# Optimization experiments

Measured on AMD Instinct MI355X. Metric: run time of the kernel, lower is better.

## Reference

```python
import jax, jax.numpy as jnp
import numpy as np

B, T = 128, 512
V, E, H, A, L = 50000, 256, 512, 64, 2


def setup_inputs() -> dict:
    key = jax.random.key(0)
    ks = jax.random.split(key, 16)
    token_ids = jax.random.randint(ks[0], (B, T), 0, V, dtype=jnp.int32)
    # lengths must be >= 2 so that the source's (len-1)-1 index is valid
    lengths = jnp.clip(jax.random.randint(ks[1], (B,), 0, T, dtype=jnp.int32), 4, T)
    s = 0.05
    inp = {
        "token_ids": token_ids,
        "lengths": lengths,
        "embedding": jax.random.normal(ks[2], (V, E), jnp.float32) * s,
        "Wt": jax.random.normal(ks[3], (A, E), jnp.float32) * s,   # tokens_linear
        "bt": jax.random.normal(ks[4], (A,), jnp.float32) * s,
        "Wq": jax.random.normal(ks[5], (A, H), jnp.float32) * s,   # query_linear
        "bq": jax.random.normal(ks[6], (A,), jnp.float32) * s,
        "v": jax.random.normal(ks[7], (A,), jnp.float32) * s,      # attention_linear weight
        "bv": jax.random.normal(ks[8], (), jnp.float32) * s,       # attention_linear bias
        "gru_Wih0": jax.random.normal(ks[9], (3 * H, A), jnp.float32) * s,
        "gru_Whh0": jax.random.normal(ks[10], (3 * H, H), jnp.float32) * s,
        "gru_bih0": jax.random.normal(ks[11], (3 * H,), jnp.float32) * s,
        "gru_bhh0": jax.random.normal(ks[12], (3 * H,), jnp.float32) * s,
        "gru_Wih1": jax.random.normal(ks[13], (3 * H, H), jnp.float32) * s,
        "gru_Whh1": jax.random.normal(ks[14], (3 * H, H), jnp.float32) * s,
        "gru_bih1": jax.random.normal(ks[15], (3 * H,), jnp.float32) * s,
        "gru_bhh1": jax.random.normal(jax.random.fold_in(key, 99), (3 * H,), jnp.float32) * s,
    }
    return inp


def _gru_cell(x, h, Wih, Whh, bih, bhh):
    gi = x @ Wih.T + bih      # [B, 3H]
    gh = h @ Whh.T + bhh      # [B, 3H]
    i_r, i_z, i_n = jnp.split(gi, 3, axis=-1)
    h_r, h_z, h_n = jnp.split(gh, 3, axis=-1)
    r = jax.nn.sigmoid(i_r + h_r)
    z = jax.nn.sigmoid(i_z + h_z)
    n = jnp.tanh(i_n + r * h_n)
    return (1.0 - z) * n + z * h


def reference(token_ids, lengths, embedding, Wt, bt, Wq, bq, v, bv,
              gru_Wih0, gru_Whh0, gru_bih0, gru_bhh0,
              gru_Wih1, gru_Whh1, gru_bih1, gru_bhh1):
    x = embedding[token_ids]                 # [B, T, E]
    tp = jnp.einsum('bte,ae->bta', x, Wt) + bt   # tokens_linear, [B, T, A]
    pos = jnp.arange(T)

    def step(h, i):
        # query = hidden_state[-1] (zeros at step 0, matching hidden_state=None)
        q = h[-1] @ Wq.T + bq                # [B, A]
        s = jnp.tanh(tp + q[:, None, :]) @ v + bv   # [B, T]
        s = jnp.where(pos[None, :] <= i, s, -jnp.inf)  # growing prefix
        attn = jax.nn.softmax(s, axis=1)
        ctx = jnp.einsum('bt,bta->ba', attn, tp)     # [B, A]
        h0 = _gru_cell(ctx, h[0], gru_Wih0, gru_Whh0, gru_bih0, gru_bhh0)
        h1 = _gru_cell(h0, h[1], gru_Wih1, gru_Whh1, gru_bih1, gru_bhh1)
        return jnp.stack([h0, h1]), h1

    h_init = jnp.zeros((L, B, H), tp.dtype)
    _, outs = jax.lax.scan(step, h_init, jnp.arange(T))   # outs: [T, B, H]
    # source: sequence_lengths = len-1, then index sequence_lengths-1 = len-2
    idx = jnp.clip(lengths - 2, 0, T - 1)
    result = outs[idx, jnp.arange(B)]                     # [B, H]
    return result
```

## Files before the change

### kernel.cpp

```cpp
#include <hip/hip_runtime.h>

#define NB 128
#define NT 512
#define NE 256
#define NH 512
#define NA 64
#define NG 8
#define GB 16

typedef short bf16x8 __attribute__((ext_vector_type(8)));
typedef float f32x4 __attribute__((ext_vector_type(4)));
typedef unsigned short u16x8 __attribute__((ext_vector_type(8)));
typedef unsigned long long u64;

__device__ __forceinline__ unsigned short f2bf(float f){
  unsigned u = __builtin_bit_cast(unsigned, f);
  u = u + 0x7fffu + ((u >> 16) & 1u);
  return (unsigned short)(u >> 16);
}
__device__ __forceinline__ float bf2f(unsigned short h){
  unsigned u = ((unsigned)h) << 16;
  return __builtin_bit_cast(float, u);
}
__device__ __forceinline__ bf16x8 packbf2(f32x4 a, f32x4 b){
  bf16x8 r;
  r[0]=(short)f2bf(a[0]); r[1]=(short)f2bf(a[1]); r[2]=(short)f2bf(a[2]); r[3]=(short)f2bf(a[3]);
  r[4]=(short)f2bf(b[0]); r[5]=(short)f2bf(b[1]); r[6]=(short)f2bf(b[2]); r[7]=(short)f2bf(b[3]);
  return r;
}
__device__ __forceinline__ bf16x8 loadB_f32(const float* p){
  f32x4 a = *(const f32x4*)p;
  f32x4 b = *(const f32x4*)(p + 4);
  return packbf2(a, b);
}
#define MFMA(a,b,c) __builtin_amdgcn_mfma_f32_16x16x32_bf16(a,b,c,0,0,0)

__device__ __forceinline__ float fsig(float x){
  return __builtin_amdgcn_rcpf(1.f + __expf(-x));
}
__device__ __forceinline__ float ftanh(float x){
  float e2 = __expf(2.f * x);
  return 1.f - 2.f * __builtin_amdgcn_rcpf(e2 + 1.f);
}

__device__ __forceinline__ void sleep_bk(int bk){
  if (bk <= 0)      __builtin_amdgcn_s_sleep(1);
  else if (bk == 1) __builtin_amdgcn_s_sleep(2);
  else if (bk == 2) __builtin_amdgcn_s_sleep(4);
  else              __builtin_amdgcn_s_sleep(8);
}

__device__ __forceinline__ u64 aload(const u64* p){
  return __hip_atomic_load(p, __ATOMIC_RELAXED, __HIP_MEMORY_SCOPE_AGENT);
}
__device__ __forceinline__ void fire(u64* p, u64 v){
  (void)__hip_atomic_exchange(p, v, __ATOMIC_RELAXED, __HIP_MEMORY_SCOPE_AGENT);
}
__device__ __forceinline__ u64 packh(unsigned sq, float a, float b){
  return ((u64)sq << 32) | ((u64)f2bf(b) << 16) | (u64)f2bf(a);
}
__device__ __forceinline__ u64 packf(unsigned sq, float a){
  return ((u64)sq << 32) | (u64)__builtin_bit_cast(unsigned, a);
}

__global__ __launch_bounds__(256) void k_tp(
    const int* __restrict__ tok, const float* __restrict__ emb,
    const float* __restrict__ Wt, const float* __restrict__ bt,
    unsigned short* __restrict__ tp)
{
  const int lane = threadIdx.x & 63;
  const int w = threadIdx.x >> 6;
  const int m16 = lane & 15, quad = lane >> 4;

  bf16x8 wfq[8][4];
#pragma unroll
  for (int kc = 0; kc < 8; kc++)
#pragma unroll
    for (int nt = 0; nt < 4; nt++)
      wfq[kc][nt] = loadB_f32(Wt + (nt*16 + m16)*NE + kc*32 + quad*8);

  float btv[4];
#pragma unroll
  for (int nt = 0; nt < 4; nt++) btv[nt] = bt[nt*16 + m16];

  const int gw = blockIdx.x * 4 + w;
#pragma unroll 1
  for (int it = 0; it < 4; it++){
    const int pt = gw * 4 + it;
    const int pos = pt*16 + m16;
    const long row = (long)tok[pos];
    const float* xrow = emb + row * NE;
    f32x4 acc[4] = {{0,0,0,0},{0,0,0,0},{0,0,0,0},{0,0,0,0}};
#pragma unroll
    for (int kc = 0; kc < 8; kc++){
      bf16x8 af = loadB_f32(xrow + kc*32 + quad*8);
#pragma unroll
      for (int nt = 0; nt < 4; nt++)
        acc[nt] = MFMA(af, wfq[kc][nt], acc[nt]);
    }
#pragma unroll
    for (int nt = 0; nt < 4; nt++)
#pragma unroll
      for (int r = 0; r < 4; r++){
        int posr = pt*16 + quad*4 + r;
        tp[(long)posr * NA + nt*16 + m16] = f2bf(acc[nt][r] + btv[nt]);
      }
  }
}

__global__ __launch_bounds__(256) void k_pack(
    const float* __restrict__ Wq, unsigned short* __restrict__ blob)
{
  const int lane = threadIdx.x & 63, wv = threadIdx.x >> 6;
  const int m16 = lane & 15, quad = lane >> 4;
#pragma unroll
  for (int kc = 0; kc < 16; kc++){
    bf16x8 t = loadB_f32(Wq + (long)(wv*16 + m16)*NH + kc*32 + quad*8);
    *(bf16x8*)&blob[((wv*16 + kc)*64 + lane)*8] = t;
  }
}

struct KArgs {
  const int* len;
  const float* bq; const float* v; const float* bv;
  const float* Wih0; const float* Whh0; const float* bih0; const float* bhh0;
  const float* Wih1; const float* Whh1; const float* bih1; const float* bhh1;
  const unsigned short* tp;
  const unsigned short* wqblob;
  u64* hbuf;
  u64* cbuf;
  float* out;
};

__device__ __forceinline__ void stage_load(const u64* __restrict__ buf, unsigned sq,
                                           unsigned short (*hs)[64][8], int tid){
  const int lane = tid & 63, wv = tid >> 6;
  const int b = lane & 15, q8 = lane >> 4;
  u64 x[16];
  int bk = 0;
  for (;;){
    bool ok = true;
#pragma unroll
    for (int c = 0; c < 4; c++){
      const u64* u0 = buf + ((wv*4 + c)*4 + q8)*64 + b*4;
#pragma unroll
      for (int j = 0; j < 4; j++) x[c*4 + j] = aload(u0 + j);
    }
#pragma unroll
    for (int t = 0; t < 16; t++) ok &= ((unsigned)(x[t] >> 32) == sq);
    if (ok) break;
    sleep_bk(bk);
    if (bk < 3) bk++;
  }
#pragma unroll
  for (int c = 0; c < 4; c++){
    u16x8 d;
#pragma unroll
    for (int j = 0; j < 4; j++){
      d[2*j]   = (unsigned short)x[c*4 + j];
      d[2*j+1] = (unsigned short)(x[c*4 + j] >> 16);
    }
    *(u16x8*)&hs[wv*4 + c][lane][0] = d;
  }
}

__global__ __launch_bounds__(256, 1) void k_main(KArgs A_)
{
  const int tid = threadIdx.x, lane = tid & 63, w = tid >> 6;
  const int g = blockIdx.x & 7, m = blockIdx.x >> 3;
  const int m16 = lane & 15, quad = lane >> 4;

  __shared__ __attribute__((aligned(16))) unsigned short h0s[16][64][8];
  __shared__ __attribute__((aligned(16))) unsigned short h1s[16][64][8];
  __shared__ __attribute__((aligned(16))) float dslab[6][256];
  __shared__ __attribute__((aligned(16))) float qs[16][68];
  __shared__ __attribute__((aligned(16))) float cslab[4][64];
  __shared__ float cden[4];
  __shared__ __attribute__((aligned(16))) unsigned short ctxf[64][16];

  u64* hb = A_.hbuf + (long)g * (4*4096);
  u64* cb = A_.cbuf + (long)g * (2*2*16*72);
  const int b0 = g * GB;

  bf16x8 wf[48], wih0f[2];
  float bhh0v[4], bih0v[4], bhh1v[4], bih1v[4];
  if (w < 3){
    const int r0 = w * NH + m * 16;
#pragma unroll
    for (int kc = 0; kc < 16; kc++){
      wf[kc]    = loadB_f32(A_.Whh0 + (long)(r0 + m16)*NH + kc*32 + quad*8);
      wf[16+kc] = loadB_f32(A_.Whh1 + (long)(r0 + m16)*NH + kc*32 + quad*8);
      wf[32+kc] = loadB_f32(A_.Wih1 + (long)(r0 + m16)*NH + kc*32 + quad*8);
    }
#pragma unroll
    for (int kc = 0; kc < 2; kc++)
      wih0f[kc] = loadB_f32(A_.Wih0 + (r0 + m16)*NA + kc*32 + quad*8);
#pragma unroll
    for (int r = 0; r < 4; r++){
      int d = r0 + quad*4 + r;
      bhh0v[r] = A_.bhh0[d]; bih0v[r] = A_.bih0[d];
      bhh1v[r] = A_.bhh1[d]; bih1v[r] = A_.bih1[d];
    }
  }
  float bqw[4];
#pragma unroll
  for (int r = 0; r < 4; r++) bqw[r] = A_.bq[w*16 + quad*4 + r];

  float vv[16];
#pragma unroll
  for (int jj = 0; jj < 16; jj++) vv[jj] = A_.v[quad*16 + jj];
  const float bvv = A_.bv[0];
  const int ab = m >> 1;
  const int wr = (m & 1)*4 + w;

  int myidx = 0, imax = 0;
#pragma unroll 1
  for (int b = 0; b < GB; b++){
    int L = A_.len[b0 + b];
    int ix = L - 2; ix = ix < 0 ? 0 : (ix > NT-1 ? NT-1 : ix);
    if (b == m16) myidx = ix;
    imax = imax > ix ? imax : ix;
  }

  f32x4 h0p = {0,0,0,0}, h1p = {0,0,0,0};

  {
    u16x8 z = {0,0,0,0,0,0,0,0};
#pragma unroll
    for (int c = 0; c < 4; c++){
      int kc = (tid>>6)*4 + c;
      *(u16x8*)&h0s[kc][lane][0] = z;
      *(u16x8*)&h1s[kc][lane][0] = z;
    }
  }
  __syncthreads();

#pragma unroll 1
  for (int i = 0; i <= imax; i++){
    const int par = i & 1;
    const unsigned sq = (unsigned)(i + 1);

    f32x4 g0 = {0,0,0,0};
    if (w < 3){
#pragma unroll
      for (int kc = 0; kc < 16; kc++){
        bf16x8 h0f = *(const bf16x8*)&h0s[kc][lane][0];
        g0 = MFMA(wf[kc], h0f, g0);
      }
#pragma unroll
      for (int r = 0; r < 4; r++) g0[r] += bhh0v[r];
    }
    if (i > 0){
      stage_load(hb + (long)(2 + ((i-1)&1))*4096, (unsigned)i, h1s, tid);
      __syncthreads();
    }
    {
      f32x4 qa = {0,0,0,0};
#pragma unroll
      for (int kc = 0; kc < 16; kc++){
        bf16x8 b1f = *(const bf16x8*)&h1s[kc][lane][0];
        bf16x8 af = *(const bf16x8*)&A_.wqblob[((w*16 + kc)*64 + lane)*8];
        qa = MFMA(af, b1f, qa);
      }
#pragma unroll
      for (int r = 0; r < 4; r++)
        qs[m16][w*16 + quad*4 + r] = qa[r] + bqw[r];
    }
    __syncthreads();

    {
      float qv[16];
#pragma unroll
      for (int jq = 0; jq < 4; jq++){
        f32x4 t = *(const f32x4*)&qs[ab][quad*16 + jq*4];
        qv[jq*4+0]=t[0]; qv[jq*4+1]=t[1]; qv[jq*4+2]=t[2]; qv[jq*4+3]=t[3];
      }
      float ctxp[16];
#pragma unroll
      for (int jj = 0; jj < 16; jj++) ctxp[jj] = 0.f;
      float denp = 0.f;
      const unsigned short* tpb = A_.tp + (long)(b0 + ab) * NT * NA;
#pragma unroll 1
      for (int c = wr; c*16 <= i; c += 8){
        const int t = c*16 + m16;
        const unsigned short* tpp = tpb + (long)t*NA + quad*16;
        u16x8 ta = *(const u16x8*)tpp;
        u16x8 tb = *(const u16x8*)(tpp + 8);
        float tpf[16];
#pragma unroll
        for (int jj = 0; jj < 8; jj++){ tpf[jj] = bf2f(ta[jj]); tpf[8+jj] = bf2f(tb[jj]); }
        float sp = 0.f;
#pragma unroll
        for (int jj = 0; jj < 16; jj++){
          float x = tpf[jj] + qv[jj];
          sp = fmaf(ftanh(x), vv[jj], sp);
        }
        sp += __shfl_xor(sp, 16);
        sp += __shfl_xor(sp, 32);
        float e = __expf(sp + bvv);
        e = (t <= i) ? e : 0.f;
        denp += e;
#pragma unroll
        for (int jj = 0; jj < 16; jj++) ctxp[jj] = fmaf(e, tpf[jj], ctxp[jj]);
      }
#pragma unroll
      for (int off = 1; off < 64; off <<= 1) denp += __shfl_xor(denp, off);
      denp *= 0.25f;
#pragma unroll
      for (int st = 0; st < 4; st++){
        const int bit = 1 << st;
        const bool up = (lane >> st) & 1;
        const int n2 = (16 >> st) >> 1;
#pragma unroll
        for (int j2 = 0; j2 < 8; j2++){
          if (j2 < n2){
            float keep = up ? ctxp[2*j2+1] : ctxp[2*j2];
            float send = up ? ctxp[2*j2]   : ctxp[2*j2+1];
            float got = __shfl_xor(send, bit);
            ctxp[j2] = keep + got;
          }
        }
      }
      cslab[w][lane] = ctxp[0];
      if (lane == 0) cden[w] = denp;
    }
    __syncthreads();
    if (w == 0){
      float s = cslab[0][lane] + cslab[1][lane] + cslab[2][lane] + cslab[3][lane];
      u64* slot = cb + ((long)(par*2 + (m & 1))*16 + ab)*72;
      fire(slot + lane, packf(sq, s));
      if (lane == 0)
        fire(slot + 64, packf(sq, cden[0]+cden[1]+cden[2]+cden[3]));
    }

    if (w == 3){
      const u64* c0 = cb + ((long)(par*2 + 0)*16 + m16)*72;
      const u64* c1 = cb + ((long)(par*2 + 1)*16 + m16)*72;
      u64 d0, d1, t0[16], t1[16];
      int bk = 0;
      for (;;){
        bool ok = true;
        d0 = aload(c0 + 64); d1 = aload(c1 + 64);
#pragma unroll
        for (int kc = 0; kc < 2; kc++){
          const int a0 = kc*32 + quad*8;
#pragma unroll
          for (int j = 0; j < 8; j++){
            t0[kc*8 + j] = aload(c0 + a0 + j);
            t1[kc*8 + j] = aload(c1 + a0 + j);
          }
        }
        ok = ((unsigned)(d0>>32) == sq) & ((unsigned)(d1>>32) == sq);
#pragma unroll
        for (int t = 0; t < 16; t++)
          ok &= ((unsigned)(t0[t]>>32) == sq) & ((unsigned)(t1[t]>>32) == sq);
        if (ok) break;
        sleep_bk(bk);
        if (bk < 3) bk++;
      }
      const float rdn = __builtin_amdgcn_rcpf(
          __builtin_bit_cast(float,(unsigned)d0) + __builtin_bit_cast(float,(unsigned)d1));
#pragma unroll
      for (int kc = 0; kc < 2; kc++){
        u16x8 f;
#pragma unroll
        for (int j = 0; j < 8; j++){
          float s = (__builtin_bit_cast(float,(unsigned)t0[kc*8+j]) +
                     __builtin_bit_cast(float,(unsigned)t1[kc*8+j])) * rdn;
          f[j] = f2bf(s);
        }
        *(u16x8*)&ctxf[lane][kc*8] = f;
      }
    }
    __syncthreads();
    if (w < 3){
      f32x4 gi0 = {0,0,0,0};
      bf16x8 cf0 = *(const bf16x8*)&ctxf[lane][0];
      bf16x8 cf1 = *(const bf16x8*)&ctxf[lane][8];
      gi0 = MFMA(wih0f[0], cf0, gi0);
      gi0 = MFMA(wih0f[1], cf1, gi0);
#pragma unroll
      for (int r = 0; r < 4; r++) gi0[r] += bih0v[r];
      *(f32x4*)&dslab[w][lane*4] = g0;
      *(f32x4*)&dslab[3+w][lane*4] = gi0;
    }
    __syncthreads();
    if (w == 3){
      f32x4 ghr = *(f32x4*)&dslab[0][lane*4];
      f32x4 ghz = *(f32x4*)&dslab[1][lane*4];
      f32x4 ghn = *(f32x4*)&dslab[2][lane*4];
      f32x4 gir = *(f32x4*)&dslab[3][lane*4];
      f32x4 giz = *(f32x4*)&dslab[4][lane*4];
      f32x4 gin = *(f32x4*)&dslab[5][lane*4];
      f32x4 hn;
#pragma unroll
      for (int r = 0; r < 4; r++){
        float rr = fsig(gir[r] + ghr[r]);
        float zz = fsig(giz[r] + ghz[r]);
        float nn = ftanh(gin[r] + rr*ghn[r]);
        hn[r] = (1.f - zz)*nn + zz*h0p[r];
      }
      h0p = hn;
      const int dp0 = m*8 + quad*2;
      u64* p0 = hb + (long)par*4096 + (dp0>>2)*64 + m16*4 + (dp0&3);
      fire(p0,     packh(sq, hn[0], hn[1]));
      fire(p0 + 1, packh(sq, hn[2], hn[3]));
    }

    f32x4 gh1 = {0,0,0,0};
    if (w < 3){
#pragma unroll
      for (int kc = 0; kc < 16; kc++){
        bf16x8 b1f = *(const bf16x8*)&h1s[kc][lane][0];
        gh1 = MFMA(wf[16+kc], b1f, gh1);
      }
#pragma unroll
      for (int r = 0; r < 4; r++) gh1[r] += bhh1v[r];
    }
    stage_load(hb + (long)par*4096, sq, h0s, tid);
    __syncthreads();
    if (w < 3){
      f32x4 gi1 = {0,0,0,0};
#pragma unroll
      for (int kc = 0; kc < 16; kc++){
        bf16x8 hf = *(const bf16x8*)&h0s[kc][lane][0];
        gi1 = MFMA(wf[32+kc], hf, gi1);
      }
#pragma unroll
      for (int r = 0; r < 4; r++) gi1[r] += bih1v[r];
      *(f32x4*)&dslab[w][lane*4] = gh1;
      *(f32x4*)&dslab[3+w][lane*4] = gi1;
    }
    __syncthreads();
    if (w == 3){
      f32x4 ghr = *(f32x4*)&dslab[0][lane*4];
      f32x4 ghz = *(f32x4*)&dslab[1][lane*4];
      f32x4 ghn = *(f32x4*)&dslab[2][lane*4];
      f32x4 gir = *(f32x4*)&dslab[3][lane*4];
      f32x4 giz = *(f32x4*)&dslab[4][lane*4];
      f32x4 gin = *(f32x4*)&dslab[5][lane*4];
      f32x4 hn;
#pragma unroll
      for (int r = 0; r < 4; r++){
        float rr = fsig(gir[r] + ghr[r]);
        float zz = fsig(giz[r] + ghz[r]);
        float nn = ftanh(gin[r] + rr*ghn[r]);
        hn[r] = (1.f - zz)*nn + zz*h1p[r];
      }
      h1p = hn;
      const int dp0 = m*8 + quad*2;
      u64* p1 = hb + (long)(2 + par)*4096 + (dp0>>2)*64 + m16*4 + (dp0&3);
      fire(p1,     packh(sq, hn[0], hn[1]));
      fire(p1 + 1, packh(sq, hn[2], hn[3]));
      if (i == myidx)
        *(f32x4*)&A_.out[(long)(b0 + m16)*NH + m*16 + quad*4] = hn;
    }
  }
}

extern "C" void kernel_launch(void* const* d_in, const int* in_sizes, int n_in,
                              void* d_out, int out_size, void* d_ws, size_t ws_size,
                              hipStream_t stream)
{
  (void)in_sizes; (void)n_in; (void)out_size; (void)ws_size;
  char* ws = (char*)d_ws;
  unsigned short* tp     = (unsigned short*)ws;
  unsigned short* wqblob = (unsigned short*)(ws + 8388608);
  u64* hbuf = (u64*)(ws + 8388608 + 65536);
  u64* cbuf = hbuf + 8 * (4*4096);

  (void)hipMemsetAsync(hbuf, 0xFF, (size_t)(8*4*4096 + 8*2*2*16*72) * sizeof(u64), stream);

  k_tp<<<dim3(256), dim3(256), 0, stream>>>(
      (const int*)d_in[0], (const float*)d_in[2], (const float*)d_in[3],
      (const float*)d_in[4], tp);
  k_pack<<<dim3(1), dim3(256), 0, stream>>>((const float*)d_in[5], wqblob);

  KArgs ka;
  ka.len  = (const int*)d_in[1];
  ka.bq   = (const float*)d_in[6];
  ka.v    = (const float*)d_in[7];  ka.bv   = (const float*)d_in[8];
  ka.Wih0 = (const float*)d_in[9];  ka.Whh0 = (const float*)d_in[10];
  ka.bih0 = (const float*)d_in[11]; ka.bhh0 = (const float*)d_in[12];
  ka.Wih1 = (const float*)d_in[13]; ka.Whh1 = (const float*)d_in[14];
  ka.bih1 = (const float*)d_in[15]; ka.bhh1 = (const float*)d_in[16];
  ka.tp = tp; ka.wqblob = wqblob;
  ka.hbuf = hbuf; ka.cbuf = cbuf;
  ka.out = (float*)d_out;

  k_main<<<dim3(256), dim3(256), 0, stream>>>(ka);
}
```

Measured before the change: 7.737 ms.

## Split each batch group into two interleaved half-batches to overlap recurrence stages

Each block now processes two half-batch sub-groups (A and B, 8 sequences each) in an interleaved software pipeline, so one sub-group's attention and cross-block exchange can overlap the other's GRU work. The layer-0 hidden matmul is moved to after the h0 exchange and computed alongside the layer-1 input matmul. Exchange buffers are resized and a simpler per-thread 8-word staging load is used. This adds more barriers per step, duplicated code and extra register pressure, and uses only half the lanes in some phases.

```diff
diff --git a/kernel.cpp b/kernel.cpp
--- a/kernel.cpp
+++ b/kernel.cpp
@@ -132,36 +132,25 @@
   float* out;
 };
 
-__device__ __forceinline__ void stage_load(const u64* __restrict__ buf, unsigned sq,
-                                           unsigned short (*hs)[64][8], int tid){
-  const int lane = tid & 63, wv = tid >> 6;
-  const int b = lane & 15, q8 = lane >> 4;
-  u64 x[16];
+__device__ __forceinline__ void stage8(const u64* __restrict__ buf, unsigned sq,
+                                       unsigned short (*hs)[64][8], int tid){
+  const u64* u0 = buf + (long)tid * 8;
+  u64 x[8];
   int bk = 0;
   for (;;){
     bool ok = true;
 #pragma unroll
-    for (int c = 0; c < 4; c++){
-      const u64* u0 = buf + ((wv*4 + c)*4 + q8)*64 + b*4;
-#pragma unroll
-      for (int j = 0; j < 4; j++) x[c*4 + j] = aload(u0 + j);
-    }
-#pragma unroll
-    for (int t = 0; t < 16; t++) ok &= ((unsigned)(x[t] >> 32) == sq);
+    for (int j = 0; j < 8; j++) x[j] = aload(u0 + j);
+#pragma unroll
+    for (int j = 0; j < 8; j++) ok &= ((unsigned)(x[j] >> 32) == sq);
     if (ok) break;
     sleep_bk(bk);
     if (bk < 3) bk++;
   }
-#pragma unroll
-  for (int c = 0; c < 4; c++){
-    u16x8 d;
-#pragma unroll
-    for (int j = 0; j < 4; j++){
-      d[2*j]   = (unsigned short)x[c*4 + j];
-      d[2*j+1] = (unsigned short)(x[c*4 + j] >> 16);
-    }
-    *(u16x8*)&hs[wv*4 + c][lane][0] = d;
-  }
+  const int kc = tid >> 4, q8 = (tid >> 2) & 3, e0 = (tid & 3) * 2;
+#pragma unroll
+  for (int b = 0; b < 8; b++)
+    *(unsigned*)&hs[kc][q8*16 + b][e0] = (unsigned)x[b];
 }
 
 __global__ __launch_bounds__(256, 1) void k_main(KArgs A_)
@@ -170,16 +159,20 @@
   const int g = blockIdx.x & 7, m = blockIdx.x >> 3;
   const int m16 = lane & 15, quad = lane >> 4;
 
-  __shared__ __attribute__((aligned(16))) unsigned short h0s[16][64][8];
-  __shared__ __attribute__((aligned(16))) unsigned short h1s[16][64][8];
+  __shared__ __attribute__((aligned(16))) unsigned short h0sA[16][64][8];
+  __shared__ __attribute__((aligned(16))) unsigned short h1sA[16][64][8];
+  __shared__ __attribute__((aligned(16))) unsigned short h0sB[16][64][8];
+  __shared__ __attribute__((aligned(16))) unsigned short h1sB[16][64][8];
   __shared__ __attribute__((aligned(16))) float dslab[6][256];
   __shared__ __attribute__((aligned(16))) float qs[16][68];
   __shared__ __attribute__((aligned(16))) float cslab[4][64];
   __shared__ float cden[4];
   __shared__ __attribute__((aligned(16))) unsigned short ctxf[64][16];
 
-  u64* hb = A_.hbuf + (long)g * (4*4096);
-  u64* cb = A_.cbuf + (long)g * (2*2*16*72);
+  u64* hbA = A_.hbuf + ((long)g*2 + 0) * (4*2048);
+  u64* hbB = A_.hbuf + ((long)g*2 + 1) * (4*2048);
+  u64* cbA = A_.cbuf + ((long)g*2 + 0) * (2*2*16*72);
+  u64* cbB = A_.cbuf + ((long)g*2 + 1) * (2*2*16*72);
   const int b0 = g * GB;
 
   bf16x8 wf[48], wih0f[2];
@@ -210,27 +203,35 @@
 #pragma unroll
   for (int jj = 0; jj < 16; jj++) vv[jj] = A_.v[quad*16 + jj];
   const float bvv = A_.bv[0];
-  const int ab = m >> 1;
+  const int abl = (m >> 1) & 7;
   const int wr = (m & 1)*4 + w;
-
-  int myidx = 0, imax = 0;
+  const bool ownA = (m < 16), ownB = (m >= 16);
+
+  int myidxA = 0, myidxB = 0, imax = 0;
 #pragma unroll 1
   for (int b = 0; b < GB; b++){
     int L = A_.len[b0 + b];
     int ix = L - 2; ix = ix < 0 ? 0 : (ix > NT-1 ? NT-1 : ix);
-    if (b == m16) myidx = ix;
+    if (b == m16)     myidxA = ix;
+    if (b == m16 + 8) myidxB = ix;
     imax = imax > ix ? imax : ix;
   }
 
-  f32x4 h0p = {0,0,0,0}, h1p = {0,0,0,0};
+  f32x4 h0pA = {0,0,0,0}, h1pA = {0,0,0,0};
+  f32x4 h0pB = {0,0,0,0}, h1pB = {0,0,0,0};
+  f32x4 gh0cA = {0,0,0,0}, gh0cB = {0,0,0,0};
+  if (w < 3){
+#pragma unroll
+    for (int r = 0; r < 4; r++){ gh0cA[r] = bhh0v[r]; gh0cB[r] = bhh0v[r]; }
+  }
 
   {
     u16x8 z = {0,0,0,0,0,0,0,0};
 #pragma unroll
     for (int c = 0; c < 4; c++){
-      int kc = (tid>>6)*4 + c;
-      *(u16x8*)&h0s[kc][lane][0] = z;
-      *(u16x8*)&h1s[kc][lane][0] = z;
+      int kc = w*4 + c;
+      *(u16x8*)&h0sA[kc][lane][0] = z; *(u16x8*)&h1sA[kc][lane][0] = z;
+      *(u16x8*)&h0sB[kc][lane][0] = z; *(u16x8*)&h1sB[kc][lane][0] = z;
     }
   }
   __syncthreads();
@@ -239,26 +240,15 @@
   for (int i = 0; i <= imax; i++){
     const int par = i & 1;
     const unsigned sq = (unsigned)(i + 1);
-
-    f32x4 g0 = {0,0,0,0};
-    if (w < 3){
+    f32x4 gh1A = {0,0,0,0}, gh1B = {0,0,0,0};
+
+    if (i > 0) stage8(hbA + (long)(2 + ((i-1)&1))*2048, (unsigned)i, h1sA, tid);
+    __syncthreads();
+    if (ownA){
+      f32x4 qa = {0,0,0,0};
 #pragma unroll
       for (int kc = 0; kc < 16; kc++){
-        bf16x8 h0f = *(const bf16x8*)&h0s[kc][lane][0];
-        g0 = MFMA(wf[kc], h0f, g0);
-      }
-#pragma unroll
-      for (int r = 0; r < 4; r++) g0[r] += bhh0v[r];
-    }
-    if (i > 0){
-      stage_load(hb + (long)(2 + ((i-1)&1))*4096, (unsigned)i, h1s, tid);
-      __syncthreads();
-    }
-    {
-      f32x4 qa = {0,0,0,0};
-#pragma unroll
-      for (int kc = 0; kc < 16; kc++){
-        bf16x8 b1f = *(const bf16x8*)&h1s[kc][lane][0];
+        bf16x8 b1f = *(const bf16x8*)&h1sA[kc][lane][0];
         bf16x8 af = *(const bf16x8*)&A_.wqblob[((w*16 + kc)*64 + lane)*8];
         qa = MFMA(af, b1f, qa);
       }
@@ -267,19 +257,18 @@
         qs[m16][w*16 + quad*4 + r] = qa[r] + bqw[r];
     }
     __syncthreads();
-
-    {
+    if (ownA){
       float qv[16];
 #pragma unroll
       for (int jq = 0; jq < 4; jq++){
-        f32x4 t = *(const f32x4*)&qs[ab][quad*16 + jq*4];
+        f32x4 t = *(const f32x4*)&qs[abl][quad*16 + jq*4];
         qv[jq*4+0]=t[0]; qv[jq*4+1]=t[1]; qv[jq*4+2]=t[2]; qv[jq*4+3]=t[3];
       }
       float ctxp[16];
 #pragma unroll
       for (int jj = 0; jj < 16; jj++) ctxp[jj] = 0.f;
       float denp = 0.f;
-      const unsigned short* tpb = A_.tp + (long)(b0 + ab) * NT * NA;
+      const unsigned short* tpb = A_.tp + (long)(b0 + abl) * NT * NA;
 #pragma unroll 1
       for (int c = wr; c*16 <= i; c += 8){
         const int t = c*16 + m16;
@@ -325,17 +314,115 @@
       if (lane == 0) cden[w] = denp;
     }
     __syncthreads();
-    if (w == 0){
+    if (ownA && w == 0){
       float s = cslab[0][lane] + cslab[1][lane] + cslab[2][lane] + cslab[3][lane];
-      u64* slot = cb + ((long)(par*2 + (m & 1))*16 + ab)*72;
+      u64* slot = cbA + ((long)(par*2 + (m & 1))*16 + abl)*72;
       fire(slot + lane, packf(sq, s));
       if (lane == 0)
         fire(slot + 64, packf(sq, cden[0]+cden[1]+cden[2]+cden[3]));
     }
-
-    if (w == 3){
-      const u64* c0 = cb + ((long)(par*2 + 0)*16 + m16)*72;
-      const u64* c1 = cb + ((long)(par*2 + 1)*16 + m16)*72;
+    if (w < 3){
+#pragma unroll
+      for (int kc = 0; kc < 16; kc++){
+        bf16x8 b1f = *(const bf16x8*)&h1sA[kc][lane][0];
+        gh1A = MFMA(wf[16+kc], b1f, gh1A);
+      }
+#pragma unroll
+      for (int r = 0; r < 4; r++) gh1A[r] += bhh1v[r];
+    }
+
+    if (i > 0) stage8(hbB + (long)(2 + ((i-1)&1))*2048, (unsigned)i, h1sB, tid);
+    __syncthreads();
+    if (ownB){
+      f32x4 qa = {0,0,0,0};
+#pragma unroll
+      for (int kc = 0; kc < 16; kc++){
+        bf16x8 b1f = *(const bf16x8*)&h1sB[kc][lane][0];
+        bf16x8 af = *(const bf16x8*)&A_.wqblob[((w*16 + kc)*64 + lane)*8];
+        qa = MFMA(af, b1f, qa);
+      }
+#pragma unroll
+      for (int r = 0; r < 4; r++)
+        qs[m16][w*16 + quad*4 + r] = qa[r] + bqw[r];
+    }
+    __syncthreads();
+    if (ownB){
+      float qv[16];
+#pragma unroll
+      for (int jq = 0; jq < 4; jq++){
+        f32x4 t = *(const f32x4*)&qs[abl][quad*16 + jq*4];
+        qv[jq*4+0]=t[0]; qv[jq*4+1]=t[1]; qv[jq*4+2]=t[2]; qv[jq*4+3]=t[3];
+      }
+      float ctxp[16];
+#pragma unroll
+      for (int jj = 0; jj < 16; jj++) ctxp[jj] = 0.f;
+      float denp = 0.f;
+      const unsigned short* tpb = A_.tp + (long)(b0 + 8 + abl) * NT * NA;
+#pragma unroll 1
+      for (int c = wr; c*16 <= i; c += 8){
+        const int t = c*16 + m16;
+        const unsigned short* tpp = tpb + (long)t*NA + quad*16;
+        u16x8 ta = *(const u16x8*)tpp;
+        u16x8 tb = *(const u16x8*)(tpp + 8);
+        float tpf[16];
+#pragma unroll
+        for (int jj = 0; jj < 8; jj++){ tpf[jj] = bf2f(ta[jj]); tpf[8+jj] = bf2f(tb[jj]); }
+        float sp = 0.f;
+#pragma unroll
+        for (int jj = 0; jj < 16; jj++){
+          float x = tpf[jj] + qv[jj];
+          sp = fmaf(ftanh(x), vv[jj], sp);
+        }
+        sp += __shfl_xor(sp, 16);
+        sp += __shfl_xor(sp, 32);
+        float e = __expf(sp + bvv);
+        e = (t <= i) ? e : 0.f;
+        denp += e;
+#pragma unroll
+        for (int jj = 0; jj < 16; jj++) ctxp[jj] = fmaf(e, tpf[jj], ctxp[jj]);
+      }
+#pragma unroll
+      for (int off = 1; off < 64; off <<= 1) denp += __shfl_xor(denp, off);
+      denp *= 0.25f;
+#pragma unroll
+      for (int st = 0; st < 4; st++){
+        const int bit = 1 << st;
+        const bool up = (lane >> st) & 1;
+        const int n2 = (16 >> st) >> 1;
+#pragma unroll
+        for (int j2 = 0; j2 < 8; j2++){
+          if (j2 < n2){
+            float keep = up ? ctxp[2*j2+1] : ctxp[2*j2];
+            float send = up ? ctxp[2*j2]   : ctxp[2*j2+1];
+            float got = __shfl_xor(send, bit);
+            ctxp[j2] = keep + got;
+          }
+        }
+      }
+      cslab[w][lane] = ctxp[0];
+      if (lane == 0) cden[w] = denp;
+    }
+    __syncthreads();
+    if (ownB && w == 0){
+      float s = cslab[0][lane] + cslab[1][lane] + cslab[2][lane] + cslab[3][lane];
+      u64* slot = cbB + ((long)(par*2 + (m & 1))*16 + abl)*72;
+      fire(slot + lane, packf(sq, s));
+      if (lane == 0)
+        fire(slot + 64, packf(sq, cden[0]+cden[1]+cden[2]+cden[3]));
+    }
+    if (w < 3){
+#pragma unroll
+      for (int kc = 0; kc < 16; kc++){
+        bf16x8 b1f = *(const bf16x8*)&h1sB[kc][lane][0];
+        gh1B = MFMA(wf[16+kc], b1f, gh1B);
+      }
+#pragma unroll
+      for (int r = 0; r < 4; r++) gh1B[r] += bhh1v[r];
+    }
+
+    if (w == 3 && m16 < 8){
+      const u64* c0 = cbA + ((long)(par*2 + 0)*16 + m16)*72;
+      const u64* c1 = cbA + ((long)(par*2 + 1)*16 + m16)*72;
       u64 d0, d1, t0[16], t1[16];
       int bk = 0;
       for (;;){
@@ -381,7 +468,7 @@
       gi0 = MFMA(wih0f[1], cf1, gi0);
 #pragma unroll
       for (int r = 0; r < 4; r++) gi0[r] += bih0v[r];
-      *(f32x4*)&dslab[w][lane*4] = g0;
+      *(f32x4*)&dslab[w][lane*4] = gh0cA;
       *(f32x4*)&dslab[3+w][lane*4] = gi0;
     }
     __syncthreads();
@@ -398,38 +485,66 @@
         float rr = fsig(gir[r] + ghr[r]);
         float zz = fsig(giz[r] + ghz[r]);
         float nn = ftanh(gin[r] + rr*ghn[r]);
-        hn[r] = (1.f - zz)*nn + zz*h0p[r];
-      }
-      h0p = hn;
-      const int dp0 = m*8 + quad*2;
-      u64* p0 = hb + (long)par*4096 + (dp0>>2)*64 + m16*4 + (dp0&3);
-      fire(p0,     packh(sq, hn[0], hn[1]));
-      fire(p0 + 1, packh(sq, hn[2], hn[3]));
-    }
-
-    f32x4 gh1 = {0,0,0,0};
+        hn[r] = (1.f - zz)*nn + zz*h0pA[r];
+      }
+      h0pA = hn;
+      if (m16 < 8){
+        const int dp0 = m*8 + quad*2;
+        fire(hbA + (long)par*2048 + (long)dp0*8 + m16,     packh(sq, hn[0], hn[1]));
+        fire(hbA + (long)par*2048 + (long)(dp0+1)*8 + m16, packh(sq, hn[2], hn[3]));
+      }
+    }
+
+    if (w == 3 && m16 < 8){
+      const u64* c0 = cbB + ((long)(par*2 + 0)*16 + m16)*72;
+      const u64* c1 = cbB + ((long)(par*2 + 1)*16 + m16)*72;
+      u64 d0, d1, t0[16], t1[16];
+      int bk = 0;
+      for (;;){
+        bool ok = true;
+        d0 = aload(c0 + 64); d1 = aload(c1 + 64);
+#pragma unroll
+        for (int kc = 0; kc < 2; kc++){
+          const int a0 = kc*32 + quad*8;
+#pragma unroll
+          for (int j = 0; j < 8; j++){
+            t0[kc*8 + j] = aload(c0 + a0 + j);
+            t1[kc*8 + j] = aload(c1 + a0 + j);
+          }
+        }
+        ok = ((unsigned)(d0>>32) == sq) & ((unsigned)(d1>>32) == sq);
+#pragma unroll
+        for (int t = 0; t < 16; t++)
+          ok &= ((unsigned)(t0[t]>>32) == sq) & ((unsigned)(t1[t]>>32) == sq);
+        if (ok) break;
+        sleep_bk(bk);
+        if (bk < 3) bk++;
+      }
+      const float rdn = __builtin_amdgcn_rcpf(
+          __builtin_bit_cast(float,(unsigned)d0) + __builtin_bit_cast(float,(unsigned)d1));
+#pragma unroll
+      for (int kc = 0; kc < 2; kc++){
+        u16x8 f;
+#pragma unroll
+        for (int j = 0; j < 8; j++){
+          float s = (__builtin_bit_cast(float,(unsigned)t0[kc*8+j]) +
+                     __builtin_bit_cast(float,(unsigned)t1[kc*8+j])) * rdn;
+          f[j] = f2bf(s);
+        }
+        *(u16x8*)&ctxf[lane][kc*8] = f;
+      }
+    }
+    __syncthreads();
     if (w < 3){
-#pragma unroll
-      for (int kc = 0; kc < 16; kc++){
-        bf16x8 b1f = *(const bf16x8*)&h1s[kc][lane][0];
-        gh1 = MFMA(wf[16+kc], b1f, gh1);
-      }
-#pragma unroll
-      for (int r = 0; r < 4; r++) gh1[r] += bhh1v[r];
-    }
-    stage_load(hb + (long)par*4096, sq, h0s, tid);
-    __syncthreads();
-    if (w < 3){
-      f32x4 gi1 = {0,0,0,0};
-#pragma unroll
-      for (int kc = 0; kc < 16; kc++){
-        bf16x8 hf = *(const bf16x8*)&h0s[kc][lane][0];
-        gi1 = MFMA(wf[32+kc], hf, gi1);
-      }
-#pragma unroll
-      for (int r = 0; r < 4; r++) gi1[r] += bih1v[r];
-      *(f32x4*)&dslab[w][lane*4] = gh1;
-      *(f32x4*)&dslab[3+w][lane*4] = gi1;
+      f32x4 gi0 = {0,0,0,0};
+      bf16x8 cf0 = *(const bf16x8*)&ctxf[lane][0];
+      bf16x8 cf1 = *(const bf16x8*)&ctxf[lane][8];
+      gi0 = MFMA(wih0f[0], cf0, gi0);
+      gi0 = MFMA(wih0f[1], cf1, gi0);
+#pragma unroll
+      for (int r = 0; r < 4; r++) gi0[r] += bih0v[r];
+      *(f32x4*)&dslab[w][lane*4] = gh0cB;
+      *(f32x4*)&dslab[3+w][lane*4] = gi0;
     }
     __syncthreads();
     if (w == 3){
@@ -445,15 +560,96 @@
         float rr = fsig(gir[r] + ghr[r]);
         float zz = fsig(giz[r] + ghz[r]);
         float nn = ftanh(gin[r] + rr*ghn[r]);
-        hn[r] = (1.f - zz)*nn + zz*h1p[r];
-      }
-      h1p = hn;
-      const int dp0 = m*8 + quad*2;
-      u64* p1 = hb + (long)(2 + par)*4096 + (dp0>>2)*64 + m16*4 + (dp0&3);
-      fire(p1,     packh(sq, hn[0], hn[1]));
-      fire(p1 + 1, packh(sq, hn[2], hn[3]));
-      if (i == myidx)
-        *(f32x4*)&A_.out[(long)(b0 + m16)*NH + m*16 + quad*4] = hn;
+        hn[r] = (1.f - zz)*nn + zz*h0pB[r];
+      }
+      h0pB = hn;
+      if (m16 < 8){
+        const int dp0 = m*8 + quad*2;
+        fire(hbB + (long)par*2048 + (long)dp0*8 + m16,     packh(sq, hn[0], hn[1]));
+        fire(hbB + (long)par*2048 + (long)(dp0+1)*8 + m16, packh(sq, hn[2], hn[3]));
+      }
+    }
+
+    stage8(hbA + (long)par*2048, sq, h0sA, tid);
+    __syncthreads();
+    if (w < 3){
+      f32x4 gi1 = {0,0,0,0}, g0 = {0,0,0,0};
+#pragma unroll
+      for (int kc = 0; kc < 16; kc++){
+        bf16x8 hf = *(const bf16x8*)&h0sA[kc][lane][0];
+        gi1 = MFMA(wf[32+kc], hf, gi1);
+        g0  = MFMA(wf[kc],    hf, g0);
+      }
+#pragma unroll
+      for (int r = 0; r < 4; r++){ gi1[r] += bih1v[r]; gh0cA[r] = g0[r] + bhh0v[r]; }
+      *(f32x4*)&dslab[w][lane*4] = gh1A;
+      *(f32x4*)&dslab[3+w][lane*4] = gi1;
+    }
+    __syncthreads();
+    if (w == 3){
+      f32x4 ghr = *(f32x4*)&dslab[0][lane*4];
+      f32x4 ghz = *(f32x4*)&dslab[1][lane*4];
+      f32x4 ghn = *(f32x4*)&dslab[2][lane*4];
+      f32x4 gir = *(f32x4*)&dslab[3][lane*4];
+      f32x4 giz = *(f32x4*)&dslab[4][lane*4];
+      f32x4 gin = *(f32x4*)&dslab[5][lane*4];
+      f32x4 hn;
+#pragma unroll
+      for (int r = 0; r < 4; r++){
+        float rr = fsig(gir[r] + ghr[r]);
+        float zz = fsig(giz[r] + ghz[r]);
+        float nn = ftanh(gin[r] + rr*ghn[r]);
+        hn[r] = (1.f - zz)*nn + zz*h1pA[r];
+      }
+      h1pA = hn;
+      if (m16 < 8){
+        const int dp0 = m*8 + quad*2;
+        fire(hbA + (long)(2+par)*2048 + (long)dp0*8 + m16,     packh(sq, hn[0], hn[1]));
+        fire(hbA + (long)(2+par)*2048 + (long)(dp0+1)*8 + m16, packh(sq, hn[2], hn[3]));
+        if (i == myidxA)
+          *(f32x4*)&A_.out[(long)(b0 + m16)*NH + m*16 + quad*4] = hn;
+      }
+    }
+
+    stage8(hbB + (long)par*2048, sq, h0sB, tid);
+    __syncthreads();
+    if (w < 3){
+      f32x4 gi1 = {0,0,0,0}, g0 = {0,0,0,0};
+#pragma unroll
+      for (int kc = 0; kc < 16; kc++){
+        bf16x8 hf = *(const bf16x8*)&h0sB[kc][lane][0];
+        gi1 = MFMA(wf[32+kc], hf, gi1);
+        g0  = MFMA(wf[kc],    hf, g0);
+      }
+#pragma unroll
+      for (int r = 0; r < 4; r++){ gi1[r] += bih1v[r]; gh0cB[r] = g0[r] + bhh0v[r]; }
+      *(f32x4*)&dslab[w][lane*4] = gh1B;
+      *(f32x4*)&dslab[3+w][lane*4] = gi1;
+    }
+    __syncthreads();
+    if (w == 3){
+      f32x4 ghr = *(f32x4*)&dslab[0][lane*4];
+      f32x4 ghz = *(f32x4*)&dslab[1][lane*4];
+      f32x4 ghn = *(f32x4*)&dslab[2][lane*4];
+      f32x4 gir = *(f32x4*)&dslab[3][lane*4];
+      f32x4 giz = *(f32x4*)&dslab[4][lane*4];
+      f32x4 gin = *(f32x4*)&dslab[5][lane*4];
+      f32x4 hn;
+#pragma unroll
+      for (int r = 0; r < 4; r++){
+        float rr = fsig(gir[r] + ghr[r]);
+        float zz = fsig(giz[r] + ghz[r]);
+        float nn = ftanh(gin[r] + rr*ghn[r]);
+        hn[r] = (1.f - zz)*nn + zz*h1pB[r];
+      }
+      h1pB = hn;
+      if (m16 < 8){
+        const int dp0 = m*8 + quad*2;
+        fire(hbB + (long)(2+par)*2048 + (long)dp0*8 + m16,     packh(sq, hn[0], hn[1]));
+        fire(hbB + (long)(2+par)*2048 + (long)(dp0+1)*8 + m16, packh(sq, hn[2], hn[3]));
+        if (i == myidxB)
+          *(f32x4*)&A_.out[(long)(b0 + 8 + m16)*NH + m*16 + quad*4] = hn;
+      }
     }
   }
 }
@@ -467,9 +663,10 @@
   unsigned short* tp     = (unsigned short*)ws;
   unsigned short* wqblob = (unsigned short*)(ws + 8388608);
   u64* hbuf = (u64*)(ws + 8388608 + 65536);
-  u64* cbuf = hbuf + 8 * (4*4096);
-
-  (void)hipMemsetAsync(hbuf, 0xFF, (size_t)(8*4*4096 + 8*2*2*16*72) * sizeof(u64), stream);
+  u64* cbuf = hbuf + 8 * 2 * (4*2048);
+
+  (void)hipMemsetAsync(hbuf, 0xFF,
+      (size_t)(8*2*4*2048 + 8*2*2*2*16*72) * sizeof(u64), stream);
 
   k_tp<<<dim3(256), dim3(256), 0, stream>>>(
       (const int*)d_in[0], (const float*)d_in[2], (const float*)d_in[3],
```

New measurement: 6.781 ms. 1.14x faster.

## Split batch into 16 groups of 8 rows, doubling persistent grid to 512 blocks

Applied to the files above, without the earlier changes.

Reduces the batch group size from 16 to 8 so that there are 16 independent groups, launching 512 persistent blocks instead of 256, and repacks the exchanged hidden-state buffer so each thread stages 8 contiguous words. Only half of the blocks in each group (owner) compute the attention context, and MFMA tiles run with half of the batch columns unused. The goal is shorter per-step cross-block synchronisation chains and more CUs in use per timestep. The risks are wasted MFMA work on padded columns and whether 512 one-block-per-CU persistent blocks can all be co-resident for the spin-wait protocol.

```diff
diff --git a/kernel.cpp b/kernel.cpp
--- a/kernel.cpp
+++ b/kernel.cpp
@@ -5,8 +5,7 @@
 #define NE 256
 #define NH 512
 #define NA 64
-#define NG 8
-#define GB 16
+#define GB 8
 
 typedef short bf16x8 __attribute__((ext_vector_type(8)));
 typedef float f32x4 __attribute__((ext_vector_type(4)));
@@ -132,42 +131,33 @@
   float* out;
 };
 
-__device__ __forceinline__ void stage_load(const u64* __restrict__ buf, unsigned sq,
-                                           unsigned short (*hs)[64][8], int tid){
-  const int lane = tid & 63, wv = tid >> 6;
-  const int b = lane & 15, q8 = lane >> 4;
-  u64 x[16];
+__device__ __forceinline__ void stage8(const u64* __restrict__ buf, unsigned sq,
+                                       unsigned short (*hs)[64][8], int tid){
+  const u64* u0 = buf + (long)tid * 8;
+  u64 x[8];
   int bk = 0;
   for (;;){
     bool ok = true;
 #pragma unroll
-    for (int c = 0; c < 4; c++){
-      const u64* u0 = buf + ((wv*4 + c)*4 + q8)*64 + b*4;
-#pragma unroll
-      for (int j = 0; j < 4; j++) x[c*4 + j] = aload(u0 + j);
-    }
-#pragma unroll
-    for (int t = 0; t < 16; t++) ok &= ((unsigned)(x[t] >> 32) == sq);
+    for (int j = 0; j < 8; j++) x[j] = aload(u0 + j);
+#pragma unroll
+    for (int j = 0; j < 8; j++) ok &= ((unsigned)(x[j] >> 32) == sq);
     if (ok) break;
     sleep_bk(bk);
     if (bk < 3) bk++;
   }
-#pragma unroll
-  for (int c = 0; c < 4; c++){
-    u16x8 d;
-#pragma unroll
-    for (int j = 0; j < 4; j++){
-      d[2*j]   = (unsigned short)x[c*4 + j];
-      d[2*j+1] = (unsigned short)(x[c*4 + j] >> 16);
-    }
-    *(u16x8*)&hs[wv*4 + c][lane][0] = d;
-  }
+  const int kc = tid >> 4, q8 = (tid >> 2) & 3, e0 = (tid & 3) * 2;
+#pragma unroll
+  for (int b = 0; b < 8; b++)
+    *(unsigned*)&hs[kc][q8*16 + b][e0] = (unsigned)x[b];
 }
 
 __global__ __launch_bounds__(256, 1) void k_main(KArgs A_)
 {
   const int tid = threadIdx.x, lane = tid & 63, w = tid >> 6;
-  const int g = blockIdx.x & 7, m = blockIdx.x >> 3;
+  const int k = blockIdx.x;
+  const int gid = (k & 7) | ((k >> 8) << 3);
+  const int m = (k >> 3) & 31;
   const int m16 = lane & 15, quad = lane >> 4;
 
   __shared__ __attribute__((aligned(16))) unsigned short h0s[16][64][8];
@@ -178,9 +168,9 @@
   __shared__ float cden[4];
   __shared__ __attribute__((aligned(16))) unsigned short ctxf[64][16];
 
-  u64* hb = A_.hbuf + (long)g * (4*4096);
-  u64* cb = A_.cbuf + (long)g * (2*2*16*72);
-  const int b0 = g * GB;
+  u64* hb = A_.hbuf + (long)gid * (4*2048);
+  u64* cb = A_.cbuf + (long)gid * (2*2*GB*72);
+  const int b0 = gid * GB;
 
   bf16x8 wf[48], wih0f[2];
   float bhh0v[4], bih0v[4], bhh1v[4], bih1v[4];
@@ -210,7 +200,8 @@
 #pragma unroll
   for (int jj = 0; jj < 16; jj++) vv[jj] = A_.v[quad*16 + jj];
   const float bvv = A_.bv[0];
-  const int ab = m >> 1;
+  const bool owner = (m < 16);
+  const int ab = (m >> 1) & 7;
   const int wr = (m & 1)*4 + w;
 
   int myidx = 0, imax = 0;
@@ -228,10 +219,11 @@
     u16x8 z = {0,0,0,0,0,0,0,0};
 #pragma unroll
     for (int c = 0; c < 4; c++){
-      int kc = (tid>>6)*4 + c;
+      int kc = w*4 + c;
       *(u16x8*)&h0s[kc][lane][0] = z;
       *(u16x8*)&h1s[kc][lane][0] = z;
     }
+    if (w == 0){ *(u16x8*)&ctxf[lane][0] = z; *(u16x8*)&ctxf[lane][8] = z; }
   }
   __syncthreads();
 
@@ -251,10 +243,10 @@
       for (int r = 0; r < 4; r++) g0[r] += bhh0v[r];
     }
     if (i > 0){
-      stage_load(hb + (long)(2 + ((i-1)&1))*4096, (unsigned)i, h1s, tid);
+      stage8(hb + (long)(2 + ((i-1)&1))*2048, (unsigned)i, h1s, tid);
       __syncthreads();
     }
-    {
+    if (owner){
       f32x4 qa = {0,0,0,0};
 #pragma unroll
       for (int kc = 0; kc < 16; kc++){
@@ -268,7 +260,7 @@
     }
     __syncthreads();
 
-    {
+    if (owner){
       float qv[16];
 #pragma unroll
       for (int jq = 0; jq < 4; jq++){
@@ -325,17 +317,17 @@
       if (lane == 0) cden[w] = denp;
     }
     __syncthreads();
-    if (w == 0){
+    if (owner && w == 0){
       float s = cslab[0][lane] + cslab[1][lane] + cslab[2][lane] + cslab[3][lane];
-      u64* slot = cb + ((long)(par*2 + (m & 1))*16 + ab)*72;
+      u64* slot = cb + ((long)(par*2 + (m & 1))*GB + ab)*72;
       fire(slot + lane, packf(sq, s));
       if (lane == 0)
         fire(slot + 64, packf(sq, cden[0]+cden[1]+cden[2]+cden[3]));
     }
 
-    if (w == 3){
-      const u64* c0 = cb + ((long)(par*2 + 0)*16 + m16)*72;
-      const u64* c1 = cb + ((long)(par*2 + 1)*16 + m16)*72;
+    if (w == 3 && m16 < GB){
+      const u64* c0 = cb + ((long)(par*2 + 0)*GB + m16)*72;
+      const u64* c1 = cb + ((long)(par*2 + 1)*GB + m16)*72;
       u64 d0, d1, t0[16], t1[16];
       int bk = 0;
       for (;;){
@@ -401,10 +393,11 @@
         hn[r] = (1.f - zz)*nn + zz*h0p[r];
       }
       h0p = hn;
-      const int dp0 = m*8 + quad*2;
-      u64* p0 = hb + (long)par*4096 + (dp0>>2)*64 + m16*4 + (dp0&3);
-      fire(p0,     packh(sq, hn[0], hn[1]));
-      fire(p0 + 1, packh(sq, hn[2], hn[3]));
+      if (m16 < GB){
+        const int dp0 = m*8 + quad*2;
+        fire(hb + (long)par*2048 + (long)dp0*8 + m16,     packh(sq, hn[0], hn[1]));
+        fire(hb + (long)par*2048 + (long)(dp0+1)*8 + m16, packh(sq, hn[2], hn[3]));
+      }
     }
 
     f32x4 gh1 = {0,0,0,0};
@@ -417,7 +410,7 @@
 #pragma unroll
       for (int r = 0; r < 4; r++) gh1[r] += bhh1v[r];
     }
-    stage_load(hb + (long)par*4096, sq, h0s, tid);
+    stage8(hb + (long)par*2048, sq, h0s, tid);
     __syncthreads();
     if (w < 3){
       f32x4 gi1 = {0,0,0,0};
@@ -448,12 +441,13 @@
         hn[r] = (1.f - zz)*nn + zz*h1p[r];
       }
       h1p = hn;
-      const int dp0 = m*8 + quad*2;
-      u64* p1 = hb + (long)(2 + par)*4096 + (dp0>>2)*64 + m16*4 + (dp0&3);
-      fire(p1,     packh(sq, hn[0], hn[1]));
-      fire(p1 + 1, packh(sq, hn[2], hn[3]));
-      if (i == myidx)
-        *(f32x4*)&A_.out[(long)(b0 + m16)*NH + m*16 + quad*4] = hn;
+      if (m16 < GB){
+        const int dp0 = m*8 + quad*2;
+        fire(hb + (long)(2+par)*2048 + (long)dp0*8 + m16,     packh(sq, hn[0], hn[1]));
+        fire(hb + (long)(2+par)*2048 + (long)(dp0+1)*8 + m16, packh(sq, hn[2], hn[3]));
+        if (i == myidx)
+          *(f32x4*)&A_.out[(long)(b0 + m16)*NH + m*16 + quad*4] = hn;
+      }
     }
   }
 }
@@ -467,9 +461,10 @@
   unsigned short* tp     = (unsigned short*)ws;
   unsigned short* wqblob = (unsigned short*)(ws + 8388608);
   u64* hbuf = (u64*)(ws + 8388608 + 65536);
-  u64* cbuf = hbuf + 8 * (4*4096);
-
-  (void)hipMemsetAsync(hbuf, 0xFF, (size_t)(8*4*4096 + 8*2*2*16*72) * sizeof(u64), stream);
+  u64* cbuf = hbuf + 16 * (4*2048);
+
+  (void)hipMemsetAsync(hbuf, 0xFF,
+      (size_t)(16*4*2048 + 16*2*2*GB*72) * sizeof(u64), stream);
 
   k_tp<<<dim3(256), dim3(256), 0, stream>>>(
       (const int*)d_in[0], (const float*)d_in[2], (const float*)d_in[3],
@@ -488,5 +483,5 @@
   ka.hbuf = hbuf; ka.cbuf = cbuf;
   ka.out = (float*)d_out;
 
-  k_main<<<dim3(256), dim3(256), 0, stream>>>(ka);
-}
+  k_main<<<dim3(512), dim3(256), 0, stream>>>(ka);
+}
```

Result: slower. 12.23 ms (+58.1%).
